# Kernel tuning notes

Measured on AMD Instinct MI355X. Metric: run time of the kernel, lower is better.

The kernel has to match this reference:

```python
import jax, jax.numpy as jnp
import numpy as np

EPS = 1e-5
NEG_SLOPE = 0.01


def _bn_eval(x, gamma, beta, mean, var):
    # x: [B, C, T], per-channel inference batchnorm
    inv = jax.lax.rsqrt(var + EPS)
    return gamma[:, None] * (x - mean[:, None]) * inv[:, None] + beta[:, None]


def _spp_max(x, L, num_levels):
    """Vectorized ragged spatial pyramid max-pool.
    x: [B, C, T] (valid data for sample b lives in [0, L[b]))
    L: [B] int effective lengths (= orig_len - shift)
    Level lvl has W=2**lvl windows: window j covers [j*floor(L/W), j*floor(L/W)+ceil(L/W)),
    matching F.max_pool1d(kernel=ceil(L/W), stride=floor(L/W)).
    Output layout per torch .view(e): channel-major -> [B, C*W] per level, levels concatenated.
    """
    B, C, T = x.shape
    t = jnp.arange(T)
    outs = []
    for lvl in range(num_levels):
        W = 2 ** lvl
        s = L // W                      # stride  = floor(L / 2^lvl)
        k = (L + W - 1) // W            # kernel  = ceil(L / 2^lvl)
        j = jnp.arange(W)
        start = j[None, :] * s[:, None]                        # [B, W]
        end = jnp.minimum(start + k[:, None], L[:, None])      # [B, W]
        m = (t[None, None, :] >= start[:, :, None]) & (t[None, None, :] < end[:, :, None])  # [B, W, T]
        vals = jnp.where(m[:, :, None, :], x[:, None, :, :], -jnp.inf)  # [B, W, C, T]
        pooled = vals.max(axis=-1)                             # [B, W, C]
        outs.append(pooled.transpose(0, 2, 1).reshape(B, C * W))
    return jnp.concatenate(outs, axis=1)


def setup_inputs() -> dict:
    key = jax.random.key(0)
    ks = jax.random.split(key, 8)
    B, C, T, K, n_levels, n_tasks = 32, 128, 8192, 21, 2, 2
    n_lin = 2 * C * (2 ** n_levels - 1)
    x = jax.random.normal(ks[0], (B, C, T), dtype=jnp.float32)
    orig_len = jax.random.randint(ks[1], (B,), 1024, T + 1)
    conv1_w = jax.random.normal(ks[2], (C, C, K), dtype=jnp.float32) * (1.0 / np.sqrt(C * K))
    bn1_gamma = jnp.ones((C,), jnp.float32)
    bn1_beta = jnp.zeros((C,), jnp.float32)
    bn1_mean = jax.random.normal(ks[3], (C,), dtype=jnp.float32) * 0.1
    bn1_var = jax.random.uniform(ks[4], (C,), dtype=jnp.float32, minval=0.5, maxval=1.5)
    fc_w = jax.random.normal(ks[5], (n_tasks, n_lin), dtype=jnp.float32) * (1.0 / np.sqrt(n_lin))
    fc_b = jnp.zeros((n_tasks,), jnp.float32)
    return {"x": x, "orig_len": orig_len, "conv1_w": conv1_w, "bn1_gamma": bn1_gamma,
            "bn1_beta": bn1_beta, "bn1_mean": bn1_mean, "bn1_var": bn1_var,
            "fc_w": fc_w, "fc_b": fc_b}


def reference(x, orig_len, conv1_w, bn1_gamma, bn1_beta, bn1_mean, bn1_var, fc_w, fc_b):
    K = conv1_w.shape[-1]
    n_levels = 2
    # original forward uses conv1/bn1 for BOTH branches (conv2/bn2 dead code)
    h = jax.lax.conv_general_dilated(x, conv1_w, window_strides=(1,), padding='VALID',
                                     dimension_numbers=('NCH', 'OIH', 'NCH'))  # [B, C, T-K+1]
    h = jax.nn.leaky_relu(_bn_eval(h, bn1_gamma, bn1_beta, bn1_mean, bn1_var), NEG_SLOPE)
    x1 = _spp_max(h, orig_len - (K - 1), n_levels)       # spp1: shift = K-1
    x2 = _spp_max(h, orig_len - 2 * (K - 1), n_levels)   # spp2: shift = 2*(K-1)
    feat = jnp.concatenate([x1, x2], axis=1)             # [B, 6C]
    return feat @ fc_w.T + fc_b
```

## Files before the change

kernel.cpp:

```cpp
#include <hip/hip_runtime.h>


typedef __attribute__((ext_vector_type(4))) float f32x4;
typedef __attribute__((ext_vector_type(4))) int i32x4;
typedef unsigned short u16;
typedef unsigned int u32;
typedef signed char i8;

#define T_SZ 8192
#define C_SZ 128
#define B_SZ 32
#define KW 21
#define FEAT 768
#define SX 25.4f
#define IMIN (-2147483647 - 1)

#define XT_OFF  0
#define WP_OFF  33554432u
#define BNA_OFF 33898496u
#define BNB_OFF 33899008u
#define FK_OFF  33899520u
#define PT_OFF  33997824u

__device__ __forceinline__ u32 fkey(float f) {
  u32 u = __float_as_uint(f);
  return (u & 0x80000000u) ? ~u : (u | 0x80000000u);
}
__device__ __forceinline__ float funkey(u32 k) {
  u32 u = (k & 0x80000000u) ? (k ^ 0x80000000u) : ~k;
  return __uint_as_float(u);
}

__device__ __forceinline__ i8 q8(float v) {
  v = fminf(fmaxf(v, -127.f), 127.f);
  return (i8)__float2int_rn(v);
}

__device__ __forceinline__ void gload_lds16(void* lds, const void* g) {
  __builtin_amdgcn_global_load_lds(
      (const __attribute__((address_space(1))) u32*)g,
      (__attribute__((address_space(3))) u32*)lds, 16, 0, 0);
}

__global__ void k_absmax(const float* __restrict__ W, float* __restrict__ parts) {
  const int i0 = ((int)blockIdx.x * 256 + (int)threadIdx.x) * 4;
  float m = 0.f;
#pragma unroll
  for (int j = 0; j < 4; ++j) m = fmaxf(m, fabsf(W[i0 + j]));
#pragma unroll
  for (int d = 1; d < 64; d <<= 1) m = fmaxf(m, __shfl_xor(m, d));
  if ((threadIdx.x & 63) == 0)
    parts[blockIdx.x * 4 + (threadIdx.x >> 6)] = m;
}

__device__ __forceinline__ float reduce_parts(const float* __restrict__ parts,
                                              float* lds4) {
  float m = 0.f;
  for (int i = (int)threadIdx.x; i < 1344; i += 256) m = fmaxf(m, parts[i]);
#pragma unroll
  for (int d = 1; d < 64; d <<= 1) m = fmaxf(m, __shfl_xor(m, d));
  if (((int)threadIdx.x & 63) == 0) lds4[(int)threadIdx.x >> 6] = m;
  __syncthreads();
  return fmaxf(fmaxf(lds4[0], lds4[1]), fmaxf(lds4[2], lds4[3]));
}

__global__ void k_fused(const float* __restrict__ X, const float* __restrict__ W,
                        const float* __restrict__ g, const float* __restrict__ be,
                        const float* __restrict__ mn, const float* __restrict__ vr,
                        const float* __restrict__ parts, const int* __restrict__ olen,
                        i8* __restrict__ Xt, i8* __restrict__ Wp,
                        float* __restrict__ bnA, float* __restrict__ bnB,
                        u32* __restrict__ feat) {
  __shared__ float smem[C_SZ * 65];
  const int tid = (int)threadIdx.x;
  const int bid = (int)blockIdx.x;

  if (bid < 4096) {
    const int b = bid >> 7;
    const int t0 = (bid & 127) * 64;
    const int L1 = olen[b] - (KW - 1);
    if (t0 > L1 + 278) return;
    const float* Xb = X + (size_t)b * C_SZ * T_SZ;
    {
      const int cw = tid >> 4;
      const int ch = tid & 15;
#pragma unroll
      for (int it = 0; it < 8; ++it) {
        const int ci = it * 16 + cw;
        const f32x4 v = *(const f32x4*)&Xb[(size_t)ci * T_SZ + t0 + ch * 4];
        smem[ci * 65 + ch * 4 + 0] = v.x;
        smem[ci * 65 + ch * 4 + 1] = v.y;
        smem[ci * 65 + ch * 4 + 2] = v.z;
        smem[ci * 65 + ch * 4 + 3] = v.w;
      }
    }
    __syncthreads();
    const int t = tid >> 2;
    const int q = tid & 3;
    u32 dw[8];
#pragma unroll
    for (int d = 0; d < 8; ++d) {
      u32 w = 0;
#pragma unroll
      for (int jb = 0; jb < 4; ++jb) {
        const int j = d * 4 + jb;
        const float v = smem[(q * 32 + j) * 65 + t] * SX;
        w |= ((u32)(unsigned char)q8(v)) << (jb * 8);
      }
      dw[d] = w;
    }
    u32* dst = (u32*)(Xt + ((size_t)(b * T_SZ + t0 + t)) * C_SZ + q * 32);
    *(i32x4*)(dst + 0) = (i32x4){(int)dw[0], (int)dw[1], (int)dw[2], (int)dw[3]};
    *(i32x4*)(dst + 4) = (i32x4){(int)dw[4], (int)dw[5], (int)dw[6], (int)dw[7]};
  } else if (bid == 4096) {
    const float wmax = reduce_parts(parts, smem);
    if (tid < C_SZ) {
      const float sw = 127.f / wmax;
      const float invS = 1.f / (SX * sw);
      float inv = rsqrtf(vr[tid] + 1e-5f);
      float a = g[tid] * inv;
      bnA[tid] = a * invS;
      bnB[tid] = be[tid] - a * mn[tid];
    }
    for (int i = tid; i < B_SZ * FEAT; i += 256) feat[i] = 0u;
  } else {
    const float wmax = reduce_parts(parts, smem);
    const float sw = 127.f / wmax;
    const int i = (bid - 4097) * 256 + tid;
    const int e = i & 15;
    const int lane = (i >> 4) & 63;
    const int f = (i >> 10) & 7;
    const int wr = (i >> 13) & 1;
    const int k = i >> 14;
    const int m = f & 3, ks = f >> 2;
    const int co = wr * 64 + m * 16 + (lane & 15);
    const int ci = ks * 64 + (lane >> 4) * 16 + e;
    Wp[i] = q8(W[(co * C_SZ + ci) * KW + k] * sw);
  }
}

__global__ __launch_bounds__(256, 2)
void k_conv(const i8* __restrict__ Xt, const i8* __restrict__ Wp,
            const float* __restrict__ bnA, const float* __restrict__ bnB,
            const int* __restrict__ olen, u32* __restrict__ feat) {
  __shared__ __align__(16) i8 Xs[280 * C_SZ];
  __shared__ int parti[2][4][C_SZ];

  const int tid = (int)threadIdx.x;
  const int wid = tid >> 6, lane = tid & 63;
  const int wr = wid >> 1, wc = wid & 1;
  const int l4 = lane & 15, lh = lane >> 4;
  const int b = (int)blockIdx.y;
  const int t0 = (int)blockIdx.x * 256;

  const int len = olen[b];
  const int L1 = len - (KW - 1);
  const int L2 = len - 2 * (KW - 1);
  if (t0 >= L1) return;

  const i8* wbase = Wp + ((size_t)wr << 13) + (lane << 4);
  i32x4 av[2][4];
#pragma unroll
  for (int f = 0; f < 8; ++f)
    av[f >> 2][f & 3] = *(const i32x4*)&wbase[f << 10];

  {
    const i8* xb = Xt + (size_t)b * T_SZ * C_SZ;
    for (int i = wid; i < 35; i += 4) {
      int trow = t0 + i * 8 + (lane >> 3);
      trow = trow < T_SZ ? trow : (T_SZ - 1);
      const i8* src = xb + (size_t)trow * C_SZ + (((lane & 7) ^ (trow & 7)) << 4);
      gload_lds16(&Xs[i * 1024], src);
    }
  }
  __syncthreads();

  i32x4 acc[4][8];
#pragma unroll
  for (int m = 0; m < 4; ++m)
#pragma unroll
    for (int n = 0; n < 8; ++n) acc[m][n] = (i32x4){0, 0, 0, 0};

  const int rowc = wc * 128 + l4;
#pragma unroll
  for (int k = 0; k < KW; ++k) {
    const int kn = (k + 1 < KW) ? (k + 1) : k;
    const int rowb = rowc + k;
    const i8* wbn = wbase + ((size_t)kn << 14);
#pragma unroll
    for (int ks = 0; ks < 2; ++ks) {
      const int gran = ((ks << 2) + lh) ^ (rowb & 7);
      const i8* xp = &Xs[(rowb << 7) + (gran << 4)];
      i32x4 bv[8];
#pragma unroll
      for (int n = 0; n < 8; ++n)
        bv[n] = *(const i32x4*)&xp[n << 11];
      __builtin_amdgcn_s_setprio(1);
#pragma unroll
      for (int m = 0; m < 4; ++m)
#pragma unroll
        for (int n = 0; n < 8; ++n)
          acc[m][n] = __builtin_amdgcn_mfma_i32_16x16x64_i8(
              av[ks][m], bv[n], acc[m][n], 0, 0, 0);
      __builtin_amdgcn_s_setprio(0);
#pragma unroll
      for (int m = 0; m < 4; ++m)
        av[ks][m] = *(const i32x4*)&wbn[((ks << 2) + m) << 10];
    }
  }

  int wlo[4], whi[4];
  wlo[0] = 0;       whi[0] = (L1 + 1) >> 1;
  wlo[1] = L1 >> 1; whi[1] = L1;
  wlo[2] = 0;       whi[2] = (L2 + 1) >> 1;
  wlo[3] = L2 >> 1; whi[3] = L2;

  int tg[8];
#pragma unroll
  for (int n = 0; n < 8; ++n) tg[n] = t0 + wc * 128 + n * 16 + l4;

#pragma unroll
  for (int w = 0; w < 4; ++w) {
    bool pr[8];
#pragma unroll
    for (int n = 0; n < 8; ++n) pr[n] = (tg[n] >= wlo[w]) & (tg[n] < whi[w]);
#pragma unroll
    for (int m = 0; m < 4; ++m)
#pragma unroll
      for (int r = 0; r < 4; ++r) {
        int mx = IMIN;
#pragma unroll
        for (int n = 0; n < 8; ++n)
          mx = max(mx, pr[n] ? acc[m][n][r] : IMIN);
#pragma unroll
        for (int d = 1; d < 16; d <<= 1) mx = max(mx, __shfl_xor(mx, d));
        if (l4 == 0) parti[wc][w][wr * 64 + m * 16 + lh * 4 + r] = mx;
      }
  }
  __syncthreads();
  if (tid < C_SZ) {
    const int c = tid;
    const int v1 = max(parti[0][0][c], parti[1][0][c]);
    const int v2 = max(parti[0][1][c], parti[1][1][c]);
    const int v4 = max(parti[0][2][c], parti[1][2][c]);
    const int v5 = max(parti[0][3][c], parti[1][3][c]);
    const int v0 = max(v1, v2);
    const int v3 = max(v4, v5);
    const float a = bnA[c], bb = bnB[c];
    u32* fb_ = feat + b * FEAT;
    float h;
    h = a * (float)v0 + bb; h = h > 0.f ? h : 0.01f * h;
    atomicMax(&fb_[c], fkey(h));
    h = a * (float)v1 + bb; h = h > 0.f ? h : 0.01f * h;
    atomicMax(&fb_[128 + 2 * c], fkey(h));
    h = a * (float)v2 + bb; h = h > 0.f ? h : 0.01f * h;
    atomicMax(&fb_[129 + 2 * c], fkey(h));
    h = a * (float)v3 + bb; h = h > 0.f ? h : 0.01f * h;
    atomicMax(&fb_[384 + c], fkey(h));
    h = a * (float)v4 + bb; h = h > 0.f ? h : 0.01f * h;
    atomicMax(&fb_[512 + 2 * c], fkey(h));
    h = a * (float)v5 + bb; h = h > 0.f ? h : 0.01f * h;
    atomicMax(&fb_[513 + 2 * c], fkey(h));
  }
}

__global__ void k_fc(const u32* __restrict__ feat, const float* __restrict__ fw,
                     const float* __restrict__ fb, float* __restrict__ out) {
  const int bj = (int)blockIdx.x;
  const int b = bj >> 1, j = bj & 1;
  const int lane = (int)threadIdx.x;
  float s = 0.f;
  for (int i = lane; i < FEAT; i += 64)
    s += funkey(feat[b * FEAT + i]) * fw[j * FEAT + i];
#pragma unroll
  for (int d = 1; d < 64; d <<= 1) s += __shfl_xor(s, d);
  if (lane == 0) out[b * 2 + j] = s + fb[j];
}

extern "C" void kernel_launch(void* const* d_in, const int* in_sizes, int n_in,
                              void* d_out, int out_size, void* d_ws, size_t ws_size,
                              hipStream_t stream) {
  (void)in_sizes; (void)n_in; (void)out_size; (void)ws_size;
  const float* x     = (const float*)d_in[0];
  const int*   olen  = (const int*)d_in[1];
  const float* w     = (const float*)d_in[2];
  const float* gamma = (const float*)d_in[3];
  const float* beta  = (const float*)d_in[4];
  const float* mean  = (const float*)d_in[5];
  const float* var   = (const float*)d_in[6];
  const float* fw    = (const float*)d_in[7];
  const float* fb    = (const float*)d_in[8];
  float* out = (float*)d_out;

  char* ws = (char*)d_ws;
  i8*  Xt    = (i8*)(ws + XT_OFF);
  i8*  Wp    = (i8*)(ws + WP_OFF);
  float* bnA  = (float*)(ws + BNA_OFF);
  float* bnB  = (float*)(ws + BNB_OFF);
  u32* feat  = (u32*)(ws + FK_OFF);
  float* parts = (float*)(ws + PT_OFF);

  k_absmax<<<336, 256, 0, stream>>>(w, parts);
  k_fused<<<4097 + 1344, 256, 0, stream>>>(x, w, gamma, beta, mean, var, parts,
                                           olen, Xt, Wp, bnA, bnB, feat);
  k_conv<<<dim3(T_SZ / 256, B_SZ), 256, 0, stream>>>(Xt, Wp, bnA, bnB, olen, feat);
  k_fc<<<64, 64, 0, stream>>>(feat, fw, fb, out);
}
```

Measured before the change: 104.3 us.

## Schedule conv tiles from a compact worklist using a persistent grid

The setup kernel now builds a worklist of (batch, 128-row tile) entries that cover only the valid length of each sample. The conv kernel becomes a grid-stride persistent kernel of 128-thread blocks, each walking that worklist, so no blocks are launched only to exit early and ragged lengths balance better across CUs. Tiles shrink from 256 to 128 time rows, so the staging and Xt-transpose halo shrink to 152 rows. In exchange, halo overhead per output row rises, each block has fewer waves to hide latency, and the k loop is only partially unrolled (unroll 3).

```diff
diff --git a/kernel.cpp b/kernel.cpp
--- a/kernel.cpp
+++ b/kernel.cpp
@@ -21,6 +21,7 @@
 #define BNB_OFF 33899008u
 #define FK_OFF  33899520u
 #define PT_OFF  33997824u
+#define WL_OFF  34003200u
 
 __device__ __forceinline__ u32 fkey(float f) {
   u32 u = __float_as_uint(f);
@@ -70,7 +71,7 @@
                         const float* __restrict__ parts, const int* __restrict__ olen,
                         i8* __restrict__ Xt, i8* __restrict__ Wp,
                         float* __restrict__ bnA, float* __restrict__ bnB,
-                        u32* __restrict__ feat) {
+                        u32* __restrict__ feat, u32* __restrict__ wl) {
   __shared__ float smem[C_SZ * 65];
   const int tid = (int)threadIdx.x;
   const int bid = (int)blockIdx.x;
@@ -79,7 +80,7 @@
     const int b = bid >> 7;
     const int t0 = (bid & 127) * 64;
     const int L1 = olen[b] - (KW - 1);
-    if (t0 > L1 + 278) return;
+    if (t0 > L1 + 152) return;
     const float* Xb = X + (size_t)b * C_SZ * T_SZ;
     {
       const int cw = tid >> 4;
@@ -123,6 +124,22 @@
       bnB[tid] = be[tid] - a * mn[tid];
     }
     for (int i = tid; i < B_SZ * FEAT; i += 256) feat[i] = 0u;
+    __shared__ int off[B_SZ + 1];
+    if (tid == 0) {
+      int s = 0;
+      for (int b2 = 0; b2 < B_SZ; ++b2) {
+        off[b2] = s;
+        s += (olen[b2] - (KW - 1) + 127) >> 7;
+      }
+      off[B_SZ] = s;
+      wl[0] = (u32)s;
+    }
+    __syncthreads();
+    for (int b2 = 0; b2 < B_SZ; ++b2) {
+      const int n = off[b2 + 1] - off[b2];
+      for (int i = tid; i < n; i += 256)
+        wl[1 + off[b2] + i] = ((u32)b2 << 16) | (u32)i;
+    }
   } else {
     const float wmax = reduce_parts(parts, smem);
     const float sw = 127.f / wmax;
@@ -139,24 +156,18 @@
   }
 }
 
-__global__ __launch_bounds__(256, 2)
+__global__ __launch_bounds__(128, 2)
 void k_conv(const i8* __restrict__ Xt, const i8* __restrict__ Wp,
             const float* __restrict__ bnA, const float* __restrict__ bnB,
-            const int* __restrict__ olen, u32* __restrict__ feat) {
-  __shared__ __align__(16) i8 Xs[280 * C_SZ];
-  __shared__ int parti[2][4][C_SZ];
+            const int* __restrict__ olen, const u32* __restrict__ wl,
+            u32* __restrict__ feat) {
+  __shared__ __align__(16) i8 Xs[152 * C_SZ];
+  __shared__ int parti[4][C_SZ];
 
   const int tid = (int)threadIdx.x;
-  const int wid = tid >> 6, lane = tid & 63;
-  const int wr = wid >> 1, wc = wid & 1;
+  const int wr = tid >> 6, lane = tid & 63;
   const int l4 = lane & 15, lh = lane >> 4;
-  const int b = (int)blockIdx.y;
-  const int t0 = (int)blockIdx.x * 256;
-
-  const int len = olen[b];
-  const int L1 = len - (KW - 1);
-  const int L2 = len - 2 * (KW - 1);
-  if (t0 >= L1) return;
+  const int bid = (int)blockIdx.x;
 
   const i8* wbase = Wp + ((size_t)wr << 13) + (lane << 4);
   i32x4 av[2][4];
@@ -164,103 +175,112 @@
   for (int f = 0; f < 8; ++f)
     av[f >> 2][f & 3] = *(const i32x4*)&wbase[f << 10];
 
-  {
-    const i8* xb = Xt + (size_t)b * T_SZ * C_SZ;
-    for (int i = wid; i < 35; i += 4) {
-      int trow = t0 + i * 8 + (lane >> 3);
-      trow = trow < T_SZ ? trow : (T_SZ - 1);
-      const i8* src = xb + (size_t)trow * C_SZ + (((lane & 7) ^ (trow & 7)) << 4);
-      gload_lds16(&Xs[i * 1024], src);
-    }
-  }
-  __syncthreads();
-
-  i32x4 acc[4][8];
-#pragma unroll
-  for (int m = 0; m < 4; ++m)
-#pragma unroll
-    for (int n = 0; n < 8; ++n) acc[m][n] = (i32x4){0, 0, 0, 0};
-
-  const int rowc = wc * 128 + l4;
-#pragma unroll
-  for (int k = 0; k < KW; ++k) {
-    const int kn = (k + 1 < KW) ? (k + 1) : k;
-    const int rowb = rowc + k;
-    const i8* wbn = wbase + ((size_t)kn << 14);
-#pragma unroll
-    for (int ks = 0; ks < 2; ++ks) {
-      const int gran = ((ks << 2) + lh) ^ (rowb & 7);
-      const i8* xp = &Xs[(rowb << 7) + (gran << 4)];
-      i32x4 bv[8];
-#pragma unroll
-      for (int n = 0; n < 8; ++n)
-        bv[n] = *(const i32x4*)&xp[n << 11];
-      __builtin_amdgcn_s_setprio(1);
+  const int nit = (int)wl[0];
+  for (int it = bid; it < nit; it += 1024) {
+    const u32 e = wl[1 + it];
+    const int b = (int)(e >> 16);
+    const int t0 = (int)(e & 0xffffu) << 7;
+    const int len = olen[b];
+    const int L1 = len - (KW - 1);
+    const int L2 = len - 2 * (KW - 1);
+
+    {
+      const i8* xb = Xt + (size_t)b * T_SZ * C_SZ;
+      for (int i = wr; i < 19; i += 2) {
+        int trow = t0 + i * 8 + (lane >> 3);
+        trow = trow < T_SZ ? trow : (T_SZ - 1);
+        const i8* src = xb + (size_t)trow * C_SZ + (((lane & 7) ^ (trow & 7)) << 4);
+        gload_lds16(&Xs[i * 1024], src);
+      }
+    }
+    __syncthreads();
+
+    i32x4 acc[4][8];
+#pragma unroll
+    for (int m = 0; m < 4; ++m)
+#pragma unroll
+      for (int n = 0; n < 8; ++n) acc[m][n] = (i32x4){0, 0, 0, 0};
+
+#pragma unroll 3
+    for (int k = 0; k < KW; ++k) {
+      const int kn = (k + 1 < KW) ? (k + 1) : 0;
+      const int rowb = l4 + k;
+      const i8* wbn = wbase + ((size_t)kn << 14);
+#pragma unroll
+      for (int ks = 0; ks < 2; ++ks) {
+        const int gran = ((ks << 2) + lh) ^ (rowb & 7);
+        const i8* xp = &Xs[(rowb << 7) + (gran << 4)];
+        i32x4 bv[8];
+#pragma unroll
+        for (int n = 0; n < 8; ++n)
+          bv[n] = *(const i32x4*)&xp[n << 11];
+        __builtin_amdgcn_s_setprio(1);
+#pragma unroll
+        for (int m = 0; m < 4; ++m)
+#pragma unroll
+          for (int n = 0; n < 8; ++n)
+            acc[m][n] = __builtin_amdgcn_mfma_i32_16x16x64_i8(
+                av[ks][m], bv[n], acc[m][n], 0, 0, 0);
+        __builtin_amdgcn_s_setprio(0);
+#pragma unroll
+        for (int m = 0; m < 4; ++m)
+          av[ks][m] = *(const i32x4*)&wbn[((ks << 2) + m) << 10];
+      }
+    }
+
+    int wlo[4], whi[4];
+    wlo[0] = 0;       whi[0] = (L1 + 1) >> 1;
+    wlo[1] = L1 >> 1; whi[1] = L1;
+    wlo[2] = 0;       whi[2] = (L2 + 1) >> 1;
+    wlo[3] = L2 >> 1; whi[3] = L2;
+
+    int tg[8];
+#pragma unroll
+    for (int n = 0; n < 8; ++n) tg[n] = t0 + n * 16 + l4;
+
+#pragma unroll
+    for (int w = 0; w < 4; ++w) {
+      bool pr[8];
+#pragma unroll
+      for (int n = 0; n < 8; ++n) pr[n] = (tg[n] >= wlo[w]) & (tg[n] < whi[w]);
 #pragma unroll
       for (int m = 0; m < 4; ++m)
 #pragma unroll
-        for (int n = 0; n < 8; ++n)
-          acc[m][n] = __builtin_amdgcn_mfma_i32_16x16x64_i8(
-              av[ks][m], bv[n], acc[m][n], 0, 0, 0);
-      __builtin_amdgcn_s_setprio(0);
-#pragma unroll
-      for (int m = 0; m < 4; ++m)
-        av[ks][m] = *(const i32x4*)&wbn[((ks << 2) + m) << 10];
-    }
-  }
-
-  int wlo[4], whi[4];
-  wlo[0] = 0;       whi[0] = (L1 + 1) >> 1;
-  wlo[1] = L1 >> 1; whi[1] = L1;
-  wlo[2] = 0;       whi[2] = (L2 + 1) >> 1;
-  wlo[3] = L2 >> 1; whi[3] = L2;
-
-  int tg[8];
-#pragma unroll
-  for (int n = 0; n < 8; ++n) tg[n] = t0 + wc * 128 + n * 16 + l4;
-
-#pragma unroll
-  for (int w = 0; w < 4; ++w) {
-    bool pr[8];
-#pragma unroll
-    for (int n = 0; n < 8; ++n) pr[n] = (tg[n] >= wlo[w]) & (tg[n] < whi[w]);
-#pragma unroll
-    for (int m = 0; m < 4; ++m)
-#pragma unroll
-      for (int r = 0; r < 4; ++r) {
-        int mx = IMIN;
-#pragma unroll
-        for (int n = 0; n < 8; ++n)
-          mx = max(mx, pr[n] ? acc[m][n][r] : IMIN);
-#pragma unroll
-        for (int d = 1; d < 16; d <<= 1) mx = max(mx, __shfl_xor(mx, d));
-        if (l4 == 0) parti[wc][w][wr * 64 + m * 16 + lh * 4 + r] = mx;
-      }
-  }
-  __syncthreads();
-  if (tid < C_SZ) {
-    const int c = tid;
-    const int v1 = max(parti[0][0][c], parti[1][0][c]);
-    const int v2 = max(parti[0][1][c], parti[1][1][c]);
-    const int v4 = max(parti[0][2][c], parti[1][2][c]);
-    const int v5 = max(parti[0][3][c], parti[1][3][c]);
-    const int v0 = max(v1, v2);
-    const int v3 = max(v4, v5);
-    const float a = bnA[c], bb = bnB[c];
-    u32* fb_ = feat + b * FEAT;
-    float h;
-    h = a * (float)v0 + bb; h = h > 0.f ? h : 0.01f * h;
-    atomicMax(&fb_[c], fkey(h));
-    h = a * (float)v1 + bb; h = h > 0.f ? h : 0.01f * h;
-    atomicMax(&fb_[128 + 2 * c], fkey(h));
-    h = a * (float)v2 + bb; h = h > 0.f ? h : 0.01f * h;
-    atomicMax(&fb_[129 + 2 * c], fkey(h));
-    h = a * (float)v3 + bb; h = h > 0.f ? h : 0.01f * h;
-    atomicMax(&fb_[384 + c], fkey(h));
-    h = a * (float)v4 + bb; h = h > 0.f ? h : 0.01f * h;
-    atomicMax(&fb_[512 + 2 * c], fkey(h));
-    h = a * (float)v5 + bb; h = h > 0.f ? h : 0.01f * h;
-    atomicMax(&fb_[513 + 2 * c], fkey(h));
+        for (int r = 0; r < 4; ++r) {
+          int mx = IMIN;
+#pragma unroll
+          for (int n = 0; n < 8; ++n)
+            mx = max(mx, pr[n] ? acc[m][n][r] : IMIN);
+#pragma unroll
+          for (int d = 1; d < 16; d <<= 1) mx = max(mx, __shfl_xor(mx, d));
+          if (l4 == 0) parti[w][wr * 64 + m * 16 + lh * 4 + r] = mx;
+        }
+    }
+    __syncthreads();
+    {
+      const int c = tid;
+      const int v1 = parti[0][c];
+      const int v2 = parti[1][c];
+      const int v4 = parti[2][c];
+      const int v5 = parti[3][c];
+      const int v0 = max(v1, v2);
+      const int v3 = max(v4, v5);
+      const float a = bnA[c], bb = bnB[c];
+      u32* fb_ = feat + b * FEAT;
+      float h;
+      h = a * (float)v0 + bb; h = h > 0.f ? h : 0.01f * h;
+      atomicMax(&fb_[c], fkey(h));
+      h = a * (float)v1 + bb; h = h > 0.f ? h : 0.01f * h;
+      atomicMax(&fb_[128 + 2 * c], fkey(h));
+      h = a * (float)v2 + bb; h = h > 0.f ? h : 0.01f * h;
+      atomicMax(&fb_[129 + 2 * c], fkey(h));
+      h = a * (float)v3 + bb; h = h > 0.f ? h : 0.01f * h;
+      atomicMax(&fb_[384 + c], fkey(h));
+      h = a * (float)v4 + bb; h = h > 0.f ? h : 0.01f * h;
+      atomicMax(&fb_[512 + 2 * c], fkey(h));
+      h = a * (float)v5 + bb; h = h > 0.f ? h : 0.01f * h;
+      atomicMax(&fb_[513 + 2 * c], fkey(h));
+    }
   }
 }
 
@@ -299,10 +319,11 @@
   float* bnB  = (float*)(ws + BNB_OFF);
   u32* feat  = (u32*)(ws + FK_OFF);
   float* parts = (float*)(ws + PT_OFF);
+  u32* wl    = (u32*)(ws + WL_OFF);
 
   k_absmax<<<336, 256, 0, stream>>>(w, parts);
   k_fused<<<4097 + 1344, 256, 0, stream>>>(x, w, gamma, beta, mean, var, parts,
-                                           olen, Xt, Wp, bnA, bnB, feat);
-  k_conv<<<dim3(T_SZ / 256, B_SZ), 256, 0, stream>>>(Xt, Wp, bnA, bnB, olen, feat);
+                                           olen, Xt, Wp, bnA, bnB, feat, wl);
+  k_conv<<<1024, 128, 0, stream>>>(Xt, Wp, bnA, bnB, olen, wl, feat);
   k_fc<<<64, 64, 0, stream>>>(feat, fw, fb, out);
 }
```

After: 99.43 us, median of 2. 4.7% less time.
